# Optimization experiments

Measured on AMD Instinct MI355X. Metric: run time of the kernel, lower is better.

Reference implementation:

```python
import jax, jax.numpy as jnp
import numpy as np

WH = WW = 7          # window size
N_TOK = WH * WW      # 49 tokens per window
HEADS = 8
HEAD_DIM = 32
DIM = HEADS * HEAD_DIM  # 256
NW = 64              # windows per image (56x56 / 7x7)
BW = 64 * NW         # batch_images * windows = 4096


def _rel_pos_index(wh, ww):
    # Swin-style relative position index, flattened to (N*N,)
    coords = np.stack(np.meshgrid(np.arange(wh), np.arange(ww), indexing='ij'))  # (2, wh, ww)
    coords = coords.reshape(2, -1)                                               # (2, N)
    rel = coords[:, :, None] - coords[:, None, :]                                # (2, N, N)
    rel = rel.transpose(1, 2, 0).astype(np.int64)                                # (N, N, 2)
    rel[:, :, 0] += wh - 1
    rel[:, :, 1] += ww - 1
    rel[:, :, 0] *= 2 * ww - 1
    return jnp.asarray(rel.sum(-1).reshape(-1))                                  # (N*N,)

_REL_IDX = _rel_pos_index(WH, WW)


def setup_inputs() -> dict:
    key = jax.random.key(0)
    ks = jax.random.split(key, 5)
    x = jax.random.normal(ks[0], (BW, N_TOK, DIM), dtype=jnp.float32)
    mask = jnp.zeros((1, NW, 1, N_TOK, N_TOK), dtype=jnp.float32)
    w_qkv = jax.random.normal(ks[1], (DIM, 3 * HEADS * HEAD_DIM), dtype=jnp.float32) * 0.02
    b_qkv = jnp.zeros((3 * HEADS * HEAD_DIM,), dtype=jnp.float32)
    rel_table = jax.random.normal(ks[2], ((2 * WH - 1) * (2 * WW - 1), HEADS), dtype=jnp.float32) * 0.02
    w_out = jax.random.normal(ks[3], (HEADS * HEAD_DIM, DIM), dtype=jnp.float32) * 0.02
    b_out = jnp.zeros((DIM,), dtype=jnp.float32)
    return {"x": x, "mask": mask, "w_qkv": w_qkv, "b_qkv": b_qkv,
            "rel_table": rel_table, "w_out": w_out, "b_out": b_out}


def reference(x, mask, w_qkv, b_qkv, rel_table, w_out, b_out):
    bw, n, d = x.shape
    # QKV projection then split per original Rearrange:
    # 'b n (qkv h hd) -> qkv b h n hd'
    qkv = (x @ w_qkv + b_qkv).reshape(bw, n, 3, HEADS, HEAD_DIM)
    qkv = qkv.transpose(2, 0, 3, 1, 4)  # (3, bw, h, n, hd)
    q, k, v = qkv[0], qkv[1], qkv[2]
    # NOTE: original computes einsum('bnid,bnjd->bnij', k, q): a[i,j] = k_i . q_j
    a = jnp.einsum('bhid,bhjd->bhij', k, q) / jnp.sqrt(jnp.asarray(HEAD_DIM, x.dtype))
    # relative position bias: table gather then '(i j) h -> h i j'
    bias = rel_table[_REL_IDX].reshape(n, n, HEADS).transpose(2, 0, 1)  # (h, n, n)
    a = a + bias
    # mask add: '(b nW) h i j -> b nW h i j', + mask, back
    nw = mask.shape[1]
    a = a.reshape(bw // nw, nw, HEADS, n, n) + mask
    a = a.reshape(bw, HEADS, n, n)
    a = jax.nn.softmax(a, axis=-1)
    y = jnp.einsum('bhij,bhjd->bhid', a, v)        # (bw, h, n, hd)
    y = y.transpose(0, 2, 1, 3).reshape(bw, n, HEADS * HEAD_DIM)
    return y @ w_out + b_out
```

## Files before the change

kernel.cpp:

```cpp
#include <hip/hip_runtime.h>

typedef __attribute__((ext_vector_type(8))) short short8;
typedef __attribute__((ext_vector_type(4))) float f32x4;
typedef unsigned short u16;

#define NTOK 49
#define NBLK 4096

#define XF  0
#define QKP 16384
#define VTF 49152
#define MKF 65536
#define BQ  73728
#define BO  75264
#define POOL 75776

#define WS_WQT 0
#define WS_WOT 393216
#define WS_BIAS 524288

__device__ __forceinline__ u16 f2bf(float f) {
  unsigned u = __float_as_uint(f);
  return (u16)((u + 0x7fffu + ((u >> 16) & 1u)) >> 16);
}
__device__ __forceinline__ unsigned packbf(float a, float b) {
  return (unsigned)f2bf(a) | ((unsigned)f2bf(b) << 16);
}

__global__ void prep_kernel(const float* __restrict__ w_qkv,
                            const float* __restrict__ w_out,
                            const float* __restrict__ rel,
                            u16* __restrict__ wqTf,
                            u16* __restrict__ woTf,
                            float* __restrict__ biasf) {
  const int stride = gridDim.x * blockDim.x;
  const int gid = blockIdx.x * blockDim.x + threadIdx.x;
  for (int e = gid; e < 48 * 8 * 64 * 8; e += stride) {
    int eL = e & 7, ln = (e >> 3) & 63, ks = (e >> 9) & 7, ctg = e >> 12;
    int k = ks * 32 + (ln >> 4) * 8 + eL;
    int c = ctg * 16 + (ln & 15);
    wqTf[e] = f2bf(w_qkv[k * 768 + c]);
  }
  for (int e = gid; e < 16 * 8 * 64 * 8; e += stride) {
    int eL = e & 7, ln = (e >> 3) & 63, ks = (e >> 9) & 7, ctg = e >> 12;
    int k = ks * 32 + (ln >> 4) * 8 + eL;
    int c = ctg * 16 + (ln & 15);
    woTf[e] = f2bf(w_out[k * 256 + c]);
  }
  for (int e = gid; e < 8 * 16 * 64 * 4; e += stride) {
    int rg = e & 3, ln = (e >> 2) & 63, t = (e >> 8) & 15, h = e >> 12;
    int i = (t >> 2) * 16 + (ln & 15);
    int j = (t & 3) * 16 + (ln >> 4) * 4 + rg;
    float v;
    if (j >= NTOK) v = -1e30f;
    else if (i >= NTOK) v = 0.f;
    else {
      int dh = i / 7 - j / 7 + 6;
      int dw = i % 7 - j % 7 + 6;
      v = rel[(dh * 13 + dw) * 8 + h];
    }
    biasf[e] = v;
  }
}

__global__ void __launch_bounds__(512, 2) winattn_mfma(
    const float* __restrict__ x,
    const float* __restrict__ mask,
    const float* __restrict__ b_qkv,
    const float* __restrict__ b_out,
    const u16* __restrict__ wqTf,
    const u16* __restrict__ woTf,
    const float* __restrict__ biasf,
    float* __restrict__ out)
{
  __shared__ u16 pool[POOL];
  const int b = blockIdx.x, tid = threadIdx.x;
  const int lane = tid & 63, lo = lane & 15, hi = lane >> 4;
  const int w = tid >> 6;
  const f32x4 zf = {0.f, 0.f, 0.f, 0.f};
  float* mkf = (float*)(pool + MKF);
  float* bq  = (float*)(pool + BQ);
  float* bo  = (float*)(pool + BO);

  {
    const float4* xg = (const float4*)(x + (size_t)b * (NTOK * 256));
    for (int e = tid; e < 49 * 64; e += 512) {
      float4 v = xg[e];
      int r = e >> 6, c4 = (e & 63) << 2;
      int addr = (((r >> 4) * 8 + (c4 >> 5)) * 64 + ((c4 >> 3) & 3) * 16 + (r & 15)) * 8 + (c4 & 7);
      *(uint2*)&pool[XF + addr] = make_uint2(packbf(v.x, v.y), packbf(v.z, v.w));
    }
    for (int e = tid; e < 15 * 64; e += 512) {
      int r = 49 + (e >> 6), c4 = (e & 63) << 2;
      int addr = (((r >> 4) * 8 + (c4 >> 5)) * 64 + ((c4 >> 3) & 3) * 16 + (r & 15)) * 8 + (c4 & 7);
      *(uint2*)&pool[XF + addr] = make_uint2(0u, 0u);
    }
    const float* mrow = mask + (size_t)(b & 63) * (NTOK * NTOK);
    for (int e = tid; e < 4096; e += 512) {
      int rg = e & 3, l = (e >> 2) & 63, t = e >> 8;
      int i = (t >> 2) * 16 + (l & 15);
      int j = (t & 3) * 16 + (l >> 4) * 4 + rg;
      mkf[e] = (i < NTOK && j < NTOK) ? mrow[i * NTOK + j] : 0.f;
    }
    for (int e = tid; e < 768; e += 512) bq[e] = b_qkv[e];
    if (tid < 256) bo[tid] = b_out[tid];
  }
  __syncthreads();

  {
    const int ctg_[6] = {2*w, 2*w + 1, 16 + 2*w, 17 + 2*w, 32 + 2*w, 33 + 2*w};
    f32x4 acc[6][4];
    #pragma unroll
    for (int ct = 0; ct < 6; ++ct)
      #pragma unroll
      for (int rt = 0; rt < 4; ++rt) acc[ct][rt] = zf;
    #pragma unroll
    for (int ks = 0; ks < 8; ++ks) {
      short8 bx[4];
      #pragma unroll
      for (int rt = 0; rt < 4; ++rt)
        bx[rt] = *(const short8*)&pool[XF + ((rt * 8 + ks) * 64 + lane) * 8];
      #pragma unroll
      for (int ct = 0; ct < 6; ++ct) {
        short8 af = *(const short8*)&wqTf[((size_t)(ctg_[ct] * 8 + ks) * 64 + lane) * 8];
        #pragma unroll
        for (int rt = 0; rt < 4; ++rt)
          acc[ct][rt] = __builtin_amdgcn_mfma_f32_16x16x32_bf16(af, bx[rt], acc[ct][rt], 0, 0, 0);
      }
    }
    #pragma unroll
    for (int ct = 0; ct < 6; ++ct) {
      const int ctg = ctg_[ct];
      f32x4 bias = *(const f32x4*)&bq[ctg * 16 + hi * 4];
      #pragma unroll
      for (int rt = 0; rt < 4; ++rt) {
        f32x4 v = acc[ct][rt] + bias;
        if (ct < 4) {
          int hi2 = (ctg & 1) * 2 + (hi >> 1);
          int eb = (hi & 1) * 4;
          int base = QKP + w * 4096 + (ct >= 2 ? 2048 : 0);
          *(uint2*)&pool[base + (rt * 64 + hi2 * 16 + lo) * 8 + eb] =
              make_uint2(packbf(v[0], v[1]), packbf(v[2], v[3]));
        } else {
          int dblk = ctg & 1;
          int ks2 = rt >> 1;
          int hi2 = (rt & 1) * 2 + (lo >> 3);
          int e2 = lo & 7;
          int vb = VTF + w * 2048 + ((dblk * 2 + ks2) * 64 + hi2 * 16) * 8 + e2;
          pool[vb + (hi * 4 + 0) * 8] = f2bf(v[0]);
          pool[vb + (hi * 4 + 1) * 8] = f2bf(v[1]);
          pool[vb + (hi * 4 + 2) * 8] = f2bf(v[2]);
          pool[vb + (hi * 4 + 3) * 8] = f2bf(v[3]);
        }
      }
    }
  }
  __syncthreads();

  f32x4 sT[4][4];
  {
    short8 qa[4], ka[4];
    #pragma unroll
    for (int t2 = 0; t2 < 4; ++t2) {
      qa[t2] = *(const short8*)&pool[QKP + w * 4096 + (t2 * 64 + lane) * 8];
      ka[t2] = *(const short8*)&pool[QKP + w * 4096 + 2048 + (t2 * 64 + lane) * 8];
    }
    #pragma unroll
    for (int jt = 0; jt < 4; ++jt)
      #pragma unroll
      for (int it = 0; it < 4; ++it)
        sT[jt][it] = __builtin_amdgcn_mfma_f32_16x16x32_bf16(qa[jt], ka[it], zf, 0, 0, 0);
  }

  float inv[4];
  {
    const float* bh = biasf + ((size_t)w << 12);
    float rs[4] = {0.f, 0.f, 0.f, 0.f};
    #pragma unroll
    for (int jt = 0; jt < 4; ++jt) {
      #pragma unroll
      for (int it = 0; it < 4; ++it) {
        const int t = it * 4 + jt;
        f32x4 bm = *(const f32x4*)&bh[(t * 64 + lane) * 4];
        f32x4 mm = *(const f32x4*)&mkf[(t * 64 + lane) * 4];
        float p0 = __expf(fmaf(sT[jt][it][0], 0.17677669529663687f, bm[0] + mm[0]));
        float p1 = __expf(fmaf(sT[jt][it][1], 0.17677669529663687f, bm[1] + mm[1]));
        float p2 = __expf(fmaf(sT[jt][it][2], 0.17677669529663687f, bm[2] + mm[2]));
        float p3 = __expf(fmaf(sT[jt][it][3], 0.17677669529663687f, bm[3] + mm[3]));
        rs[it] += (p0 + p1) + (p2 + p3);
        int hi2 = (jt & 1) * 2 + (hi >> 1);
        int eb = (hi & 1) * 4;
        *(uint2*)&pool[QKP + w * 4096 + ((it * 2 + (jt >> 1)) * 64 + hi2 * 16 + lo) * 8 + eb] =
            make_uint2(packbf(p0, p1), packbf(p2, p3));
      }
    }
    #pragma unroll
    for (int it = 0; it < 4; ++it) {
      float r2 = rs[it] + __shfl_xor(rs[it], 16);
      float r4 = r2 + __shfl_xor(r2, 32);
      inv[it] = 1.f / r4;
    }
  }

  {
    short8 va[2][2];
    #pragma unroll
    for (int dblk = 0; dblk < 2; ++dblk)
      #pragma unroll
      for (int k2 = 0; k2 < 2; ++k2)
        va[dblk][k2] = *(const short8*)&pool[VTF + w * 2048 + ((dblk * 2 + k2) * 64 + lane) * 8];
    f32x4 ya[2][4];
    #pragma unroll
    for (int it = 0; it < 4; ++it) { ya[0][it] = zf; ya[1][it] = zf; }
    #pragma unroll
    for (int it = 0; it < 4; ++it)
      #pragma unroll
      for (int k2 = 0; k2 < 2; ++k2) {
        short8 pb = *(const short8*)&pool[QKP + w * 4096 + ((it * 2 + k2) * 64 + lane) * 8];
        ya[0][it] = __builtin_amdgcn_mfma_f32_16x16x32_bf16(va[0][k2], pb, ya[0][it], 0, 0, 0);
        ya[1][it] = __builtin_amdgcn_mfma_f32_16x16x32_bf16(va[1][k2], pb, ya[1][it], 0, 0, 0);
      }
    #pragma unroll
    for (int it = 0; it < 4; ++it) {
      #pragma unroll
      for (int dblk = 0; dblk < 2; ++dblk) {
        float y0 = ya[dblk][it][0] * inv[it];
        float y1 = ya[dblk][it][1] * inv[it];
        float y2 = ya[dblk][it][2] * inv[it];
        float y3 = ya[dblk][it][3] * inv[it];
        int hi2 = dblk * 2 + (hi >> 1);
        int eb = (hi & 1) * 4;
        *(uint2*)&pool[XF + ((it * 8 + w) * 64 + hi2 * 16 + lo) * 8 + eb] =
            make_uint2(packbf(y0, y1), packbf(y2, y3));
      }
    }
  }
  __syncthreads();

  {
    f32x4 pacc[2][4];
    #pragma unroll
    for (int ct = 0; ct < 2; ++ct)
      #pragma unroll
      for (int rt = 0; rt < 4; ++rt) pacc[ct][rt] = zf;
    #pragma unroll
    for (int ks = 0; ks < 8; ++ks) {
      short8 yb[4];
      #pragma unroll
      for (int rt = 0; rt < 4; ++rt)
        yb[rt] = *(const short8*)&pool[XF + ((rt * 8 + ks) * 64 + lane) * 8];
      #pragma unroll
      for (int ct = 0; ct < 2; ++ct) {
        short8 wf = *(const short8*)&woTf[((size_t)((w * 2 + ct) * 8 + ks) * 64 + lane) * 8];
        #pragma unroll
        for (int rt = 0; rt < 4; ++rt)
          pacc[ct][rt] = __builtin_amdgcn_mfma_f32_16x16x32_bf16(wf, yb[rt], pacc[ct][rt], 0, 0, 0);
      }
    }
    float* og = out + (size_t)b * (NTOK * 256);
    #pragma unroll
    for (int ct = 0; ct < 2; ++ct) {
      const int cb = (w * 2 + ct) * 16 + hi * 4;
      f32x4 bb = *(const f32x4*)&bo[cb];
      #pragma unroll
      for (int rt = 0; rt < 4; ++rt) {
        const int r = rt * 16 + lo;
        if (r < NTOK) {
          f32x4 vv = pacc[ct][rt] + bb;
          *(f32x4*)(og + (size_t)r * 256 + cb) = vv;
        }
      }
    }
  }
}

extern "C" void kernel_launch(void* const* d_in, const int* in_sizes, int n_in,
                              void* d_out, int out_size, void* d_ws, size_t ws_size,
                              hipStream_t stream) {
  const float *x = nullptr, *mask = nullptr, *w_qkv = nullptr, *b_qkv = nullptr,
              *rel_t = nullptr, *w_out = nullptr, *b_out = nullptr;
  for (int i = 0; i < n_in; ++i) {
    const float* p = (const float*)d_in[i];
    switch (in_sizes[i]) {
      case 4096 * 49 * 256: x = p; break;
      case 64 * 49 * 49:    mask = p; break;
      case 256 * 768:       w_qkv = p; break;
      case 768:             b_qkv = p; break;
      case 169 * 8:         rel_t = p; break;
      case 256 * 256:       w_out = p; break;
      case 256:             b_out = p; break;
    }
  }
  char* wsb = (char*)d_ws;
  u16* wqTf = (u16*)(wsb + WS_WQT);
  u16* woTf = (u16*)(wsb + WS_WOT);
  float* biasf = (float*)(wsb + WS_BIAS);

  hipLaunchKernelGGL(prep_kernel, dim3(512), dim3(256), 0, stream,
                     w_qkv, w_out, rel_t, wqTf, woTf, biasf);
  hipLaunchKernelGGL(winattn_mfma, dim3(NBLK), dim3(512), 0, stream,
                     x, mask, b_qkv, b_out, wqTf, woTf, biasf, (float*)d_out);
}
```

Baseline: 346.4 us.

## Use 16 waves per block, splitting attention by head and query-tile halves

Doubles the block to 1024 threads. The QKV projection is spread over 16 waves (3 column tiles each), and each head's attention is split across two waves by query-tile pairs. Softmax probabilities now stay in registers and are reshuffled with cross-lane shuffles instead of a round trip through LDS. The output projection also gives one column tile per wave. The aim is more parallelism per window and lower per-wave register pressure, at the cost of extra shuffle instructions and a launch-bounds request of 4 blocks of 1024 threads that the LDS use likely cannot meet.

```diff
diff --git a/kernel.cpp b/kernel.cpp
--- a/kernel.cpp
+++ b/kernel.cpp
@@ -48,7 +48,7 @@
     woTf[e] = f2bf(w_out[k * 256 + c]);
   }
   for (int e = gid; e < 8 * 16 * 64 * 4; e += stride) {
-    int rg = e & 3, ln = (e >> 2) & 63, t = (e >> 8) & 15, h = e >> 12;
+    int rg = e & 3, ln = (e >> 2) & 63, t = (e >> 8) & 15, hh = e >> 12;
     int i = (t >> 2) * 16 + (ln & 15);
     int j = (t & 3) * 16 + (ln >> 4) * 4 + rg;
     float v;
@@ -57,13 +57,13 @@
     else {
       int dh = i / 7 - j / 7 + 6;
       int dw = i % 7 - j % 7 + 6;
-      v = rel[(dh * 13 + dw) * 8 + h];
+      v = rel[(dh * 13 + dw) * 8 + hh];
     }
     biasf[e] = v;
   }
 }
 
-__global__ void __launch_bounds__(512, 2) winattn_mfma(
+__global__ void __launch_bounds__(1024, 4) winattn_mfma(
     const float* __restrict__ x,
     const float* __restrict__ mask,
     const float* __restrict__ b_qkv,
@@ -77,6 +77,8 @@
   const int b = blockIdx.x, tid = threadIdx.x;
   const int lane = tid & 63, lo = lane & 15, hi = lane >> 4;
   const int w = tid >> 6;
+  const int h = w & 7;
+  const int it0 = (w >> 3) * 2;
   const f32x4 zf = {0.f, 0.f, 0.f, 0.f};
   float* mkf = (float*)(pool + MKF);
   float* bq  = (float*)(pool + BQ);
@@ -84,34 +86,34 @@
 
   {
     const float4* xg = (const float4*)(x + (size_t)b * (NTOK * 256));
-    for (int e = tid; e < 49 * 64; e += 512) {
+    for (int e = tid; e < 49 * 64; e += 1024) {
       float4 v = xg[e];
       int r = e >> 6, c4 = (e & 63) << 2;
       int addr = (((r >> 4) * 8 + (c4 >> 5)) * 64 + ((c4 >> 3) & 3) * 16 + (r & 15)) * 8 + (c4 & 7);
       *(uint2*)&pool[XF + addr] = make_uint2(packbf(v.x, v.y), packbf(v.z, v.w));
     }
-    for (int e = tid; e < 15 * 64; e += 512) {
+    if (tid < 15 * 64) {
+      int e = tid;
       int r = 49 + (e >> 6), c4 = (e & 63) << 2;
       int addr = (((r >> 4) * 8 + (c4 >> 5)) * 64 + ((c4 >> 3) & 3) * 16 + (r & 15)) * 8 + (c4 & 7);
       *(uint2*)&pool[XF + addr] = make_uint2(0u, 0u);
     }
     const float* mrow = mask + (size_t)(b & 63) * (NTOK * NTOK);
-    for (int e = tid; e < 4096; e += 512) {
+    for (int e = tid; e < 4096; e += 1024) {
       int rg = e & 3, l = (e >> 2) & 63, t = e >> 8;
       int i = (t >> 2) * 16 + (l & 15);
       int j = (t & 3) * 16 + (l >> 4) * 4 + rg;
       mkf[e] = (i < NTOK && j < NTOK) ? mrow[i * NTOK + j] : 0.f;
     }
-    for (int e = tid; e < 768; e += 512) bq[e] = b_qkv[e];
+    if (tid < 768) bq[tid] = b_qkv[tid];
     if (tid < 256) bo[tid] = b_out[tid];
   }
   __syncthreads();
 
   {
-    const int ctg_[6] = {2*w, 2*w + 1, 16 + 2*w, 17 + 2*w, 32 + 2*w, 33 + 2*w};
-    f32x4 acc[6][4];
-    #pragma unroll
-    for (int ct = 0; ct < 6; ++ct)
+    f32x4 acc[3][4];
+    #pragma unroll
+    for (int ct = 0; ct < 3; ++ct)
       #pragma unroll
       for (int rt = 0; rt < 4; ++rt) acc[ct][rt] = zf;
     #pragma unroll
@@ -121,24 +123,25 @@
       for (int rt = 0; rt < 4; ++rt)
         bx[rt] = *(const short8*)&pool[XF + ((rt * 8 + ks) * 64 + lane) * 8];
       #pragma unroll
-      for (int ct = 0; ct < 6; ++ct) {
-        short8 af = *(const short8*)&wqTf[((size_t)(ctg_[ct] * 8 + ks) * 64 + lane) * 8];
+      for (int ct = 0; ct < 3; ++ct) {
+        short8 af = *(const short8*)&wqTf[((size_t)((3 * w + ct) * 8 + ks) * 64 + lane) * 8];
         #pragma unroll
         for (int rt = 0; rt < 4; ++rt)
           acc[ct][rt] = __builtin_amdgcn_mfma_f32_16x16x32_bf16(af, bx[rt], acc[ct][rt], 0, 0, 0);
       }
     }
     #pragma unroll
-    for (int ct = 0; ct < 6; ++ct) {
-      const int ctg = ctg_[ct];
+    for (int ct = 0; ct < 3; ++ct) {
+      const int ctg = 3 * w + ct;
+      const int head2 = (ctg & 15) >> 1;
       f32x4 bias = *(const f32x4*)&bq[ctg * 16 + hi * 4];
       #pragma unroll
       for (int rt = 0; rt < 4; ++rt) {
         f32x4 v = acc[ct][rt] + bias;
-        if (ct < 4) {
+        if (ctg < 32) {
+          int base = QKP + head2 * 4096 + (ctg >= 16 ? 2048 : 0);
           int hi2 = (ctg & 1) * 2 + (hi >> 1);
           int eb = (hi & 1) * 4;
-          int base = QKP + w * 4096 + (ct >= 2 ? 2048 : 0);
           *(uint2*)&pool[base + (rt * 64 + hi2 * 16 + lo) * 8 + eb] =
               make_uint2(packbf(v[0], v[1]), packbf(v[2], v[3]));
         } else {
@@ -146,7 +149,7 @@
           int ks2 = rt >> 1;
           int hi2 = (rt & 1) * 2 + (lo >> 3);
           int e2 = lo & 7;
-          int vb = VTF + w * 2048 + ((dblk * 2 + ks2) * 64 + hi2 * 16) * 8 + e2;
+          int vb = VTF + head2 * 2048 + ((dblk * 2 + ks2) * 64 + hi2 * 16) * 8 + e2;
           pool[vb + (hi * 4 + 0) * 8] = f2bf(v[0]);
           pool[vb + (hi * 4 + 1) * 8] = f2bf(v[1]);
           pool[vb + (hi * 4 + 2) * 8] = f2bf(v[2]);
@@ -157,49 +160,49 @@
   }
   __syncthreads();
 
-  f32x4 sT[4][4];
-  {
-    short8 qa[4], ka[4];
-    #pragma unroll
-    for (int t2 = 0; t2 < 4; ++t2) {
-      qa[t2] = *(const short8*)&pool[QKP + w * 4096 + (t2 * 64 + lane) * 8];
-      ka[t2] = *(const short8*)&pool[QKP + w * 4096 + 2048 + (t2 * 64 + lane) * 8];
-    }
-    #pragma unroll
-    for (int jt = 0; jt < 4; ++jt)
-      #pragma unroll
-      for (int it = 0; it < 4; ++it)
-        sT[jt][it] = __builtin_amdgcn_mfma_f32_16x16x32_bf16(qa[jt], ka[it], zf, 0, 0, 0);
-  }
-
-  float inv[4];
-  {
-    const float* bh = biasf + ((size_t)w << 12);
-    float rs[4] = {0.f, 0.f, 0.f, 0.f};
+  float rs0 = 0.f, rs1 = 0.f;
+  unsigned pkp[4][2][2];
+  {
+    short8 ka0 = *(const short8*)&pool[QKP + h * 4096 + 2048 + ((it0 + 0) * 64 + lane) * 8];
+    short8 ka1 = *(const short8*)&pool[QKP + h * 4096 + 2048 + ((it0 + 1) * 64 + lane) * 8];
+    const float* bh = biasf + ((size_t)h << 12);
     #pragma unroll
     for (int jt = 0; jt < 4; ++jt) {
-      #pragma unroll
-      for (int it = 0; it < 4; ++it) {
-        const int t = it * 4 + jt;
+      short8 qa = *(const short8*)&pool[QKP + h * 4096 + (jt * 64 + lane) * 8];
+      f32x4 s0 = __builtin_amdgcn_mfma_f32_16x16x32_bf16(qa, ka0, zf, 0, 0, 0);
+      f32x4 s1 = __builtin_amdgcn_mfma_f32_16x16x32_bf16(qa, ka1, zf, 0, 0, 0);
+      {
+        const int t = (it0 + 0) * 4 + jt;
         f32x4 bm = *(const f32x4*)&bh[(t * 64 + lane) * 4];
         f32x4 mm = *(const f32x4*)&mkf[(t * 64 + lane) * 4];
-        float p0 = __expf(fmaf(sT[jt][it][0], 0.17677669529663687f, bm[0] + mm[0]));
-        float p1 = __expf(fmaf(sT[jt][it][1], 0.17677669529663687f, bm[1] + mm[1]));
-        float p2 = __expf(fmaf(sT[jt][it][2], 0.17677669529663687f, bm[2] + mm[2]));
-        float p3 = __expf(fmaf(sT[jt][it][3], 0.17677669529663687f, bm[3] + mm[3]));
-        rs[it] += (p0 + p1) + (p2 + p3);
-        int hi2 = (jt & 1) * 2 + (hi >> 1);
-        int eb = (hi & 1) * 4;
-        *(uint2*)&pool[QKP + w * 4096 + ((it * 2 + (jt >> 1)) * 64 + hi2 * 16 + lo) * 8 + eb] =
-            make_uint2(packbf(p0, p1), packbf(p2, p3));
-      }
-    }
-    #pragma unroll
-    for (int it = 0; it < 4; ++it) {
-      float r2 = rs[it] + __shfl_xor(rs[it], 16);
-      float r4 = r2 + __shfl_xor(r2, 32);
-      inv[it] = 1.f / r4;
-    }
+        float p0 = __expf(fmaf(s0[0], 0.17677669529663687f, bm[0] + mm[0]));
+        float p1 = __expf(fmaf(s0[1], 0.17677669529663687f, bm[1] + mm[1]));
+        float p2 = __expf(fmaf(s0[2], 0.17677669529663687f, bm[2] + mm[2]));
+        float p3 = __expf(fmaf(s0[3], 0.17677669529663687f, bm[3] + mm[3]));
+        rs0 += (p0 + p1) + (p2 + p3);
+        pkp[jt][0][0] = packbf(p0, p1);
+        pkp[jt][0][1] = packbf(p2, p3);
+      }
+      {
+        const int t = (it0 + 1) * 4 + jt;
+        f32x4 bm = *(const f32x4*)&bh[(t * 64 + lane) * 4];
+        f32x4 mm = *(const f32x4*)&mkf[(t * 64 + lane) * 4];
+        float p0 = __expf(fmaf(s1[0], 0.17677669529663687f, bm[0] + mm[0]));
+        float p1 = __expf(fmaf(s1[1], 0.17677669529663687f, bm[1] + mm[1]));
+        float p2 = __expf(fmaf(s1[2], 0.17677669529663687f, bm[2] + mm[2]));
+        float p3 = __expf(fmaf(s1[3], 0.17677669529663687f, bm[3] + mm[3]));
+        rs1 += (p0 + p1) + (p2 + p3);
+        pkp[jt][1][0] = packbf(p0, p1);
+        pkp[jt][1][1] = packbf(p2, p3);
+      }
+    }
+  }
+  float inv0, inv1;
+  {
+    float r2 = rs0 + __shfl_xor(rs0, 16);
+    inv0 = 1.f / (r2 + __shfl_xor(r2, 32));
+    float r3 = rs1 + __shfl_xor(rs1, 16);
+    inv1 = 1.f / (r3 + __shfl_xor(r3, 32));
   }
 
   {
@@ -208,29 +211,44 @@
     for (int dblk = 0; dblk < 2; ++dblk)
       #pragma unroll
       for (int k2 = 0; k2 < 2; ++k2)
-        va[dblk][k2] = *(const short8*)&pool[VTF + w * 2048 + ((dblk * 2 + k2) * 64 + lane) * 8];
-    f32x4 ya[2][4];
-    #pragma unroll
-    for (int it = 0; it < 4; ++it) { ya[0][it] = zf; ya[1][it] = zf; }
-    #pragma unroll
-    for (int it = 0; it < 4; ++it)
+        va[dblk][k2] = *(const short8*)&pool[VTF + h * 2048 + ((dblk * 2 + k2) * 64 + lane) * 8];
+    f32x4 ya[2][2];
+    ya[0][0] = zf; ya[0][1] = zf; ya[1][0] = zf; ya[1][1] = zf;
+    const int src0 = lo + ((hi & 1) * 2) * 16;
+    const int src1 = src0 + 16;
+    const bool hiSel = (hi & 2) != 0;
+    #pragma unroll
+    for (int itL = 0; itL < 2; ++itL)
       #pragma unroll
       for (int k2 = 0; k2 < 2; ++k2) {
-        short8 pb = *(const short8*)&pool[QKP + w * 4096 + ((it * 2 + k2) * 64 + lane) * 8];
-        ya[0][it] = __builtin_amdgcn_mfma_f32_16x16x32_bf16(va[0][k2], pb, ya[0][it], 0, 0, 0);
-        ya[1][it] = __builtin_amdgcn_mfma_f32_16x16x32_bf16(va[1][k2], pb, ya[1][it], 0, 0, 0);
-      }
-    #pragma unroll
-    for (int it = 0; it < 4; ++it) {
+        unsigned a0 = (unsigned)__shfl((int)pkp[2 * k2][itL][0], src0);
+        unsigned b0 = (unsigned)__shfl((int)pkp[2 * k2 + 1][itL][0], src0);
+        unsigned a1 = (unsigned)__shfl((int)pkp[2 * k2][itL][1], src0);
+        unsigned b1 = (unsigned)__shfl((int)pkp[2 * k2 + 1][itL][1], src0);
+        unsigned a2 = (unsigned)__shfl((int)pkp[2 * k2][itL][0], src1);
+        unsigned b2 = (unsigned)__shfl((int)pkp[2 * k2 + 1][itL][0], src1);
+        unsigned a3 = (unsigned)__shfl((int)pkp[2 * k2][itL][1], src1);
+        unsigned b3 = (unsigned)__shfl((int)pkp[2 * k2 + 1][itL][1], src1);
+        union { unsigned u[4]; short8 s8; } pb;
+        pb.u[0] = hiSel ? b0 : a0;
+        pb.u[1] = hiSel ? b1 : a1;
+        pb.u[2] = hiSel ? b2 : a2;
+        pb.u[3] = hiSel ? b3 : a3;
+        ya[0][itL] = __builtin_amdgcn_mfma_f32_16x16x32_bf16(va[0][k2], pb.s8, ya[0][itL], 0, 0, 0);
+        ya[1][itL] = __builtin_amdgcn_mfma_f32_16x16x32_bf16(va[1][k2], pb.s8, ya[1][itL], 0, 0, 0);
+      }
+    #pragma unroll
+    for (int itL = 0; itL < 2; ++itL) {
+      const float inv = itL ? inv1 : inv0;
       #pragma unroll
       for (int dblk = 0; dblk < 2; ++dblk) {
-        float y0 = ya[dblk][it][0] * inv[it];
-        float y1 = ya[dblk][it][1] * inv[it];
-        float y2 = ya[dblk][it][2] * inv[it];
-        float y3 = ya[dblk][it][3] * inv[it];
+        float y0 = ya[dblk][itL][0] * inv;
+        float y1 = ya[dblk][itL][1] * inv;
+        float y2 = ya[dblk][itL][2] * inv;
+        float y3 = ya[dblk][itL][3] * inv;
         int hi2 = dblk * 2 + (hi >> 1);
         int eb = (hi & 1) * 4;
-        *(uint2*)&pool[XF + ((it * 8 + w) * 64 + hi2 * 16 + lo) * 8 + eb] =
+        *(uint2*)&pool[XF + (((it0 + itL) * 8 + h) * 64 + hi2 * 16 + lo) * 8 + eb] =
             make_uint2(packbf(y0, y1), packbf(y2, y3));
       }
     }
@@ -238,37 +256,26 @@
   __syncthreads();
 
   {
-    f32x4 pacc[2][4];
-    #pragma unroll
-    for (int ct = 0; ct < 2; ++ct)
-      #pragma unroll
-      for (int rt = 0; rt < 4; ++rt) pacc[ct][rt] = zf;
+    f32x4 pacc[4];
+    pacc[0] = zf; pacc[1] = zf; pacc[2] = zf; pacc[3] = zf;
     #pragma unroll
     for (int ks = 0; ks < 8; ++ks) {
-      short8 yb[4];
-      #pragma unroll
-      for (int rt = 0; rt < 4; ++rt)
-        yb[rt] = *(const short8*)&pool[XF + ((rt * 8 + ks) * 64 + lane) * 8];
-      #pragma unroll
-      for (int ct = 0; ct < 2; ++ct) {
-        short8 wf = *(const short8*)&woTf[((size_t)((w * 2 + ct) * 8 + ks) * 64 + lane) * 8];
-        #pragma unroll
-        for (int rt = 0; rt < 4; ++rt)
-          pacc[ct][rt] = __builtin_amdgcn_mfma_f32_16x16x32_bf16(wf, yb[rt], pacc[ct][rt], 0, 0, 0);
+      short8 wf = *(const short8*)&woTf[((size_t)(w * 8 + ks) * 64 + lane) * 8];
+      #pragma unroll
+      for (int rt = 0; rt < 4; ++rt) {
+        short8 yb = *(const short8*)&pool[XF + ((rt * 8 + ks) * 64 + lane) * 8];
+        pacc[rt] = __builtin_amdgcn_mfma_f32_16x16x32_bf16(wf, yb, pacc[rt], 0, 0, 0);
       }
     }
     float* og = out + (size_t)b * (NTOK * 256);
-    #pragma unroll
-    for (int ct = 0; ct < 2; ++ct) {
-      const int cb = (w * 2 + ct) * 16 + hi * 4;
-      f32x4 bb = *(const f32x4*)&bo[cb];
-      #pragma unroll
-      for (int rt = 0; rt < 4; ++rt) {
-        const int r = rt * 16 + lo;
-        if (r < NTOK) {
-          f32x4 vv = pacc[ct][rt] + bb;
-          *(f32x4*)(og + (size_t)r * 256 + cb) = vv;
-        }
+    const int cb = w * 16 + hi * 4;
+    f32x4 bb = *(const f32x4*)&bo[cb];
+    #pragma unroll
+    for (int rt = 0; rt < 4; ++rt) {
+      const int r = rt * 16 + lo;
+      if (r < NTOK) {
+        f32x4 vv = pacc[rt] + bb;
+        *(f32x4*)(og + (size_t)r * 256 + cb) = vv;
       }
     }
   }
@@ -298,6 +305,6 @@
 
   hipLaunchKernelGGL(prep_kernel, dim3(512), dim3(256), 0, stream,
                      w_qkv, w_out, rel_t, wqTf, woTf, biasf);
-  hipLaunchKernelGGL(winattn_mfma, dim3(NBLK), dim3(512), 0, stream,
+  hipLaunchKernelGGL(winattn_mfma, dim3(NBLK), dim3(1024), 0, stream,
                      x, mask, b_qkv, b_out, wqTf, woTf, biasf, (float*)d_out);
 }
```

Measured after the change: 290.0 us. -16.3%, faster.

## Keep Q/K/P in registers via lane shuffles and shrink LDS for higher occupancy

Applied to the files above, without the earlier changes.

Q and K stay in registers and are rearranged into MFMA operand layout with cross-lane shuffles, and the softmax probabilities are handled the same way. This removes the Q/K/P shared-memory round trips and one barrier. The per-window mask is pre-laid-out in a workspace buffer by the prep kernel, and the biases are read straight from global memory, so LDS shrinks from about 148KB to 64KB and launch bounds rise to 4 blocks per CU. In exchange it adds many shuffle instructions and puts more register pressure under the tighter occupancy target, which could cause spills.

```diff
diff --git a/kernel.cpp b/kernel.cpp
--- a/kernel.cpp
+++ b/kernel.cpp
@@ -7,17 +7,14 @@
 #define NTOK 49
 #define NBLK 4096
 
-#define XF  0
-#define QKP 16384
-#define VTF 49152
-#define MKF 65536
-#define BQ  73728
-#define BO  75264
-#define POOL 75776
+#define XF 0
+#define VY 16384
+#define POOLN 32768
 
 #define WS_WQT 0
 #define WS_WOT 393216
 #define WS_BIAS 524288
+#define WS_MKG 655360
 
 __device__ __forceinline__ u16 f2bf(float f) {
   unsigned u = __float_as_uint(f);
@@ -27,12 +24,33 @@
   return (unsigned)f2bf(a) | ((unsigned)f2bf(b) << 16);
 }
 
+__device__ __forceinline__ short8 asm_frag(unsigned c0p0, unsigned c0p1,
+                                           unsigned c1p0, unsigned c1p1,
+                                           int srcA, int srcB, bool cSel) {
+  unsigned a0 = (unsigned)__shfl((int)c0p0, srcA);
+  unsigned b0 = (unsigned)__shfl((int)c1p0, srcA);
+  unsigned a1 = (unsigned)__shfl((int)c0p1, srcA);
+  unsigned b1 = (unsigned)__shfl((int)c1p1, srcA);
+  unsigned a2 = (unsigned)__shfl((int)c0p0, srcB);
+  unsigned b2 = (unsigned)__shfl((int)c1p0, srcB);
+  unsigned a3 = (unsigned)__shfl((int)c0p1, srcB);
+  unsigned b3 = (unsigned)__shfl((int)c1p1, srcB);
+  union { unsigned u[4]; short8 s8; } r;
+  r.u[0] = cSel ? b0 : a0;
+  r.u[1] = cSel ? b1 : a1;
+  r.u[2] = cSel ? b2 : a2;
+  r.u[3] = cSel ? b3 : a3;
+  return r.s8;
+}
+
 __global__ void prep_kernel(const float* __restrict__ w_qkv,
                             const float* __restrict__ w_out,
                             const float* __restrict__ rel,
+                            const float* __restrict__ mask,
                             u16* __restrict__ wqTf,
                             u16* __restrict__ woTf,
-                            float* __restrict__ biasf) {
+                            float* __restrict__ biasf,
+                            float* __restrict__ mkg) {
   const int stride = gridDim.x * blockDim.x;
   const int gid = blockIdx.x * blockDim.x + threadIdx.x;
   for (int e = gid; e < 48 * 8 * 64 * 8; e += stride) {
@@ -48,7 +66,7 @@
     woTf[e] = f2bf(w_out[k * 256 + c]);
   }
   for (int e = gid; e < 8 * 16 * 64 * 4; e += stride) {
-    int rg = e & 3, ln = (e >> 2) & 63, t = (e >> 8) & 15, h = e >> 12;
+    int rg = e & 3, ln = (e >> 2) & 63, t = (e >> 8) & 15, hh = e >> 12;
     int i = (t >> 2) * 16 + (ln & 15);
     int j = (t & 3) * 16 + (ln >> 4) * 4 + rg;
     float v;
@@ -57,30 +75,33 @@
     else {
       int dh = i / 7 - j / 7 + 6;
       int dw = i % 7 - j % 7 + 6;
-      v = rel[(dh * 13 + dw) * 8 + h];
+      v = rel[(dh * 13 + dw) * 8 + hh];
     }
     biasf[e] = v;
   }
-}
-
-__global__ void __launch_bounds__(512, 2) winattn_mfma(
+  for (int e = gid; e < 64 * 16 * 64 * 4; e += stride) {
+    int rg = e & 3, ln = (e >> 2) & 63, t = (e >> 8) & 15, wdw = e >> 12;
+    int i = (t >> 2) * 16 + (ln & 15);
+    int j = (t & 3) * 16 + (ln >> 4) * 4 + rg;
+    mkg[e] = (i < NTOK && j < NTOK) ? mask[wdw * (NTOK * NTOK) + i * NTOK + j] : 0.f;
+  }
+}
+
+__global__ void __launch_bounds__(512, 4) winattn_mfma(
     const float* __restrict__ x,
-    const float* __restrict__ mask,
     const float* __restrict__ b_qkv,
     const float* __restrict__ b_out,
     const u16* __restrict__ wqTf,
     const u16* __restrict__ woTf,
     const float* __restrict__ biasf,
+    const float* __restrict__ mkg,
     float* __restrict__ out)
 {
-  __shared__ u16 pool[POOL];
+  __shared__ u16 pool[POOLN];
   const int b = blockIdx.x, tid = threadIdx.x;
   const int lane = tid & 63, lo = lane & 15, hi = lane >> 4;
-  const int w = tid >> 6;
+  const int h = tid >> 6;
   const f32x4 zf = {0.f, 0.f, 0.f, 0.f};
-  float* mkf = (float*)(pool + MKF);
-  float* bq  = (float*)(pool + BQ);
-  float* bo  = (float*)(pool + BO);
 
   {
     const float4* xg = (const float4*)(x + (size_t)b * (NTOK * 256));
@@ -95,23 +116,15 @@
       int addr = (((r >> 4) * 8 + (c4 >> 5)) * 64 + ((c4 >> 3) & 3) * 16 + (r & 15)) * 8 + (c4 & 7);
       *(uint2*)&pool[XF + addr] = make_uint2(0u, 0u);
     }
-    const float* mrow = mask + (size_t)(b & 63) * (NTOK * NTOK);
-    for (int e = tid; e < 4096; e += 512) {
-      int rg = e & 3, l = (e >> 2) & 63, t = e >> 8;
-      int i = (t >> 2) * 16 + (l & 15);
-      int j = (t & 3) * 16 + (l >> 4) * 4 + rg;
-      mkf[e] = (i < NTOK && j < NTOK) ? mrow[i * NTOK + j] : 0.f;
-    }
-    for (int e = tid; e < 768; e += 512) bq[e] = b_qkv[e];
-    if (tid < 256) bo[tid] = b_out[tid];
   }
   __syncthreads();
 
-  {
-    const int ctg_[6] = {2*w, 2*w + 1, 16 + 2*w, 17 + 2*w, 32 + 2*w, 33 + 2*w};
-    f32x4 acc[6][4];
-    #pragma unroll
-    for (int ct = 0; ct < 6; ++ct)
+  unsigned pq[2][4][2], pk[2][4][2];
+  {
+    const int ctgA[3] = {2 * h, 2 * h + 1, 16 + 2 * h};
+    f32x4 acc[3][4];
+    #pragma unroll
+    for (int ct = 0; ct < 3; ++ct)
       #pragma unroll
       for (int rt = 0; rt < 4; ++rt) acc[ct][rt] = zf;
     #pragma unroll
@@ -121,32 +134,58 @@
       for (int rt = 0; rt < 4; ++rt)
         bx[rt] = *(const short8*)&pool[XF + ((rt * 8 + ks) * 64 + lane) * 8];
       #pragma unroll
-      for (int ct = 0; ct < 6; ++ct) {
-        short8 af = *(const short8*)&wqTf[((size_t)(ctg_[ct] * 8 + ks) * 64 + lane) * 8];
+      for (int ct = 0; ct < 3; ++ct) {
+        short8 af = *(const short8*)&wqTf[((size_t)(ctgA[ct] * 8 + ks) * 64 + lane) * 8];
         #pragma unroll
         for (int rt = 0; rt < 4; ++rt)
           acc[ct][rt] = __builtin_amdgcn_mfma_f32_16x16x32_bf16(af, bx[rt], acc[ct][rt], 0, 0, 0);
       }
     }
     #pragma unroll
-    for (int ct = 0; ct < 6; ++ct) {
-      const int ctg = ctg_[ct];
-      f32x4 bias = *(const f32x4*)&bq[ctg * 16 + hi * 4];
+    for (int ct = 0; ct < 3; ++ct) {
+      f32x4 bias = *(const f32x4*)(b_qkv + ctgA[ct] * 16 + hi * 4);
       #pragma unroll
       for (int rt = 0; rt < 4; ++rt) {
         f32x4 v = acc[ct][rt] + bias;
-        if (ct < 4) {
-          int hi2 = (ctg & 1) * 2 + (hi >> 1);
-          int eb = (hi & 1) * 4;
-          int base = QKP + w * 4096 + (ct >= 2 ? 2048 : 0);
-          *(uint2*)&pool[base + (rt * 64 + hi2 * 16 + lo) * 8 + eb] =
-              make_uint2(packbf(v[0], v[1]), packbf(v[2], v[3]));
-        } else {
-          int dblk = ctg & 1;
-          int ks2 = rt >> 1;
+        if (ct < 2) { pq[ct][rt][0] = packbf(v[0], v[1]); pq[ct][rt][1] = packbf(v[2], v[3]); }
+        else        { pk[0][rt][0]  = packbf(v[0], v[1]); pk[0][rt][1]  = packbf(v[2], v[3]); }
+      }
+    }
+  }
+  {
+    const int ctgB[3] = {17 + 2 * h, 32 + 2 * h, 33 + 2 * h};
+    f32x4 acc[3][4];
+    #pragma unroll
+    for (int ct = 0; ct < 3; ++ct)
+      #pragma unroll
+      for (int rt = 0; rt < 4; ++rt) acc[ct][rt] = zf;
+    #pragma unroll
+    for (int ks = 0; ks < 8; ++ks) {
+      short8 bx[4];
+      #pragma unroll
+      for (int rt = 0; rt < 4; ++rt)
+        bx[rt] = *(const short8*)&pool[XF + ((rt * 8 + ks) * 64 + lane) * 8];
+      #pragma unroll
+      for (int ct = 0; ct < 3; ++ct) {
+        short8 af = *(const short8*)&wqTf[((size_t)(ctgB[ct] * 8 + ks) * 64 + lane) * 8];
+        #pragma unroll
+        for (int rt = 0; rt < 4; ++rt)
+          acc[ct][rt] = __builtin_amdgcn_mfma_f32_16x16x32_bf16(af, bx[rt], acc[ct][rt], 0, 0, 0);
+      }
+    }
+    #pragma unroll
+    for (int ct = 0; ct < 3; ++ct) {
+      f32x4 bias = *(const f32x4*)(b_qkv + ctgB[ct] * 16 + hi * 4);
+      #pragma unroll
+      for (int rt = 0; rt < 4; ++rt) {
+        f32x4 v = acc[ct][rt] + bias;
+        if (ct == 0) { pk[1][rt][0] = packbf(v[0], v[1]); pk[1][rt][1] = packbf(v[2], v[3]); }
+        else {
+          const int dblk = ct - 1;
+          int k2 = rt >> 1;
           int hi2 = (rt & 1) * 2 + (lo >> 3);
           int e2 = lo & 7;
-          int vb = VTF + w * 2048 + ((dblk * 2 + ks2) * 64 + hi2 * 16) * 8 + e2;
+          int vb = VY + ((dblk * 2 + k2) * 8 + h) * 512 + (hi2 * 16) * 8 + e2;
           pool[vb + (hi * 4 + 0) * 8] = f2bf(v[0]);
           pool[vb + (hi * 4 + 1) * 8] = f2bf(v[1]);
           pool[vb + (hi * 4 + 2) * 8] = f2bf(v[2]);
@@ -155,83 +194,70 @@
       }
     }
   }
-  __syncthreads();
-
-  f32x4 sT[4][4];
-  {
-    short8 qa[4], ka[4];
-    #pragma unroll
-    for (int t2 = 0; t2 < 4; ++t2) {
-      qa[t2] = *(const short8*)&pool[QKP + w * 4096 + (t2 * 64 + lane) * 8];
-      ka[t2] = *(const short8*)&pool[QKP + w * 4096 + 2048 + (t2 * 64 + lane) * 8];
-    }
-    #pragma unroll
-    for (int jt = 0; jt < 4; ++jt)
-      #pragma unroll
-      for (int it = 0; it < 4; ++it)
-        sT[jt][it] = __builtin_amdgcn_mfma_f32_16x16x32_bf16(qa[jt], ka[it], zf, 0, 0, 0);
-  }
-
-  float inv[4];
-  {
-    const float* bh = biasf + ((size_t)w << 12);
-    float rs[4] = {0.f, 0.f, 0.f, 0.f};
+
+  const int srcA = lo + 32 * (hi & 1);
+  const int srcB = srcA + 16;
+  const bool cSel = hi >= 2;
+  unsigned pkp[4][4][2];
+  float rs[4] = {0.f, 0.f, 0.f, 0.f};
+  {
+    short8 ka[4];
+    #pragma unroll
+    for (int it = 0; it < 4; ++it)
+      ka[it] = asm_frag(pk[0][it][0], pk[0][it][1], pk[1][it][0], pk[1][it][1], srcA, srcB, cSel);
+    const float* bh = biasf + h * 4096;
+    const float* mh = mkg + (size_t)(b & 63) * 4096;
     #pragma unroll
     for (int jt = 0; jt < 4; ++jt) {
+      short8 qa = asm_frag(pq[0][jt][0], pq[0][jt][1], pq[1][jt][0], pq[1][jt][1], srcA, srcB, cSel);
       #pragma unroll
       for (int it = 0; it < 4; ++it) {
+        f32x4 st = __builtin_amdgcn_mfma_f32_16x16x32_bf16(qa, ka[it], zf, 0, 0, 0);
         const int t = it * 4 + jt;
         f32x4 bm = *(const f32x4*)&bh[(t * 64 + lane) * 4];
-        f32x4 mm = *(const f32x4*)&mkf[(t * 64 + lane) * 4];
-        float p0 = __expf(fmaf(sT[jt][it][0], 0.17677669529663687f, bm[0] + mm[0]));
-        float p1 = __expf(fmaf(sT[jt][it][1], 0.17677669529663687f, bm[1] + mm[1]));
-        float p2 = __expf(fmaf(sT[jt][it][2], 0.17677669529663687f, bm[2] + mm[2]));
-        float p3 = __expf(fmaf(sT[jt][it][3], 0.17677669529663687f, bm[3] + mm[3]));
+        f32x4 mm = *(const f32x4*)&mh[(t * 64 + lane) * 4];
+        float p0 = __expf(fmaf(st[0], 0.17677669529663687f, bm[0] + mm[0]));
+        float p1 = __expf(fmaf(st[1], 0.17677669529663687f, bm[1] + mm[1]));
+        float p2 = __expf(fmaf(st[2], 0.17677669529663687f, bm[2] + mm[2]));
+        float p3 = __expf(fmaf(st[3], 0.17677669529663687f, bm[3] + mm[3]));
         rs[it] += (p0 + p1) + (p2 + p3);
-        int hi2 = (jt & 1) * 2 + (hi >> 1);
-        int eb = (hi & 1) * 4;
-        *(uint2*)&pool[QKP + w * 4096 + ((it * 2 + (jt >> 1)) * 64 + hi2 * 16 + lo) * 8 + eb] =
-            make_uint2(packbf(p0, p1), packbf(p2, p3));
-      }
-    }
+        pkp[jt][it][0] = packbf(p0, p1);
+        pkp[jt][it][1] = packbf(p2, p3);
+      }
+    }
+  }
+  float inv[4];
+  #pragma unroll
+  for (int it = 0; it < 4; ++it) {
+    float r2 = rs[it] + __shfl_xor(rs[it], 16);
+    inv[it] = 1.f / (r2 + __shfl_xor(r2, 32));
+  }
+
+  {
+    short8 va[2][2];
+    #pragma unroll
+    for (int dblk = 0; dblk < 2; ++dblk)
+      #pragma unroll
+      for (int k2 = 0; k2 < 2; ++k2)
+        va[dblk][k2] = *(const short8*)&pool[VY + ((dblk * 2 + k2) * 8 + h) * 512 + lane * 8];
     #pragma unroll
     for (int it = 0; it < 4; ++it) {
-      float r2 = rs[it] + __shfl_xor(rs[it], 16);
-      float r4 = r2 + __shfl_xor(r2, 32);
-      inv[it] = 1.f / r4;
-    }
-  }
-
-  {
-    short8 va[2][2];
-    #pragma unroll
-    for (int dblk = 0; dblk < 2; ++dblk)
-      #pragma unroll
-      for (int k2 = 0; k2 < 2; ++k2)
-        va[dblk][k2] = *(const short8*)&pool[VTF + w * 2048 + ((dblk * 2 + k2) * 64 + lane) * 8];
-    f32x4 ya[2][4];
-    #pragma unroll
-    for (int it = 0; it < 4; ++it) { ya[0][it] = zf; ya[1][it] = zf; }
-    #pragma unroll
-    for (int it = 0; it < 4; ++it)
+      f32x4 y0 = zf, y1 = zf;
       #pragma unroll
       for (int k2 = 0; k2 < 2; ++k2) {
-        short8 pb = *(const short8*)&pool[QKP + w * 4096 + ((it * 2 + k2) * 64 + lane) * 8];
-        ya[0][it] = __builtin_amdgcn_mfma_f32_16x16x32_bf16(va[0][k2], pb, ya[0][it], 0, 0, 0);
-        ya[1][it] = __builtin_amdgcn_mfma_f32_16x16x32_bf16(va[1][k2], pb, ya[1][it], 0, 0, 0);
-      }
-    #pragma unroll
-    for (int it = 0; it < 4; ++it) {
+        short8 pb = asm_frag(pkp[2 * k2][it][0], pkp[2 * k2][it][1],
+                             pkp[2 * k2 + 1][it][0], pkp[2 * k2 + 1][it][1], srcA, srcB, cSel);
+        y0 = __builtin_amdgcn_mfma_f32_16x16x32_bf16(va[0][k2], pb, y0, 0, 0, 0);
+        y1 = __builtin_amdgcn_mfma_f32_16x16x32_bf16(va[1][k2], pb, y1, 0, 0, 0);
+      }
+      const float iv = inv[it];
       #pragma unroll
       for (int dblk = 0; dblk < 2; ++dblk) {
-        float y0 = ya[dblk][it][0] * inv[it];
-        float y1 = ya[dblk][it][1] * inv[it];
-        float y2 = ya[dblk][it][2] * inv[it];
-        float y3 = ya[dblk][it][3] * inv[it];
+        f32x4 yy = dblk ? y1 : y0;
         int hi2 = dblk * 2 + (hi >> 1);
         int eb = (hi & 1) * 4;
-        *(uint2*)&pool[XF + ((it * 8 + w) * 64 + hi2 * 16 + lo) * 8 + eb] =
-            make_uint2(packbf(y0, y1), packbf(y2, y3));
+        *(uint2*)&pool[VY + (it * 8 + h) * 512 + (hi2 * 16 + lo) * 8 + eb] =
+            make_uint2(packbf(yy[0] * iv, yy[1] * iv), packbf(yy[2] * iv, yy[3] * iv));
       }
     }
   }
@@ -248,10 +274,10 @@
       short8 yb[4];
       #pragma unroll
       for (int rt = 0; rt < 4; ++rt)
-        yb[rt] = *(const short8*)&pool[XF + ((rt * 8 + ks) * 64 + lane) * 8];
+        yb[rt] = *(const short8*)&pool[VY + (rt * 8 + ks) * 512 + lane * 8];
       #pragma unroll
       for (int ct = 0; ct < 2; ++ct) {
-        short8 wf = *(const short8*)&woTf[((size_t)((w * 2 + ct) * 8 + ks) * 64 + lane) * 8];
+        short8 wf = *(const short8*)&woTf[((size_t)((h * 2 + ct) * 8 + ks) * 64 + lane) * 8];
         #pragma unroll
         for (int rt = 0; rt < 4; ++rt)
           pacc[ct][rt] = __builtin_amdgcn_mfma_f32_16x16x32_bf16(wf, yb[rt], pacc[ct][rt], 0, 0, 0);
@@ -260,8 +286,8 @@
     float* og = out + (size_t)b * (NTOK * 256);
     #pragma unroll
     for (int ct = 0; ct < 2; ++ct) {
-      const int cb = (w * 2 + ct) * 16 + hi * 4;
-      f32x4 bb = *(const f32x4*)&bo[cb];
+      const int cb = (h * 2 + ct) * 16 + hi * 4;
+      f32x4 bb = *(const f32x4*)(b_out + cb);
       #pragma unroll
       for (int rt = 0; rt < 4; ++rt) {
         const int r = rt * 16 + lo;
@@ -292,12 +318,13 @@
     }
   }
   char* wsb = (char*)d_ws;
-  u16* wqTf = (u16*)(wsb + WS_WQT);
-  u16* woTf = (u16*)(wsb + WS_WOT);
+  u16* wqTf   = (u16*)(wsb + WS_WQT);
+  u16* woTf   = (u16*)(wsb + WS_WOT);
   float* biasf = (float*)(wsb + WS_BIAS);
-
-  hipLaunchKernelGGL(prep_kernel, dim3(512), dim3(256), 0, stream,
-                     w_qkv, w_out, rel_t, wqTf, woTf, biasf);
+  float* mkg   = (float*)(wsb + WS_MKG);
+
+  hipLaunchKernelGGL(prep_kernel, dim3(1024), dim3(256), 0, stream,
+                     w_qkv, w_out, rel_t, mask, wqTf, woTf, biasf, mkg);
   hipLaunchKernelGGL(winattn_mfma, dim3(NBLK), dim3(512), 0, stream,
-                     x, mask, b_qkv, b_out, wqTf, woTf, biasf, (float*)d_out);
-}
+                     x, b_qkv, b_out, wqTf, woTf, biasf, mkg, (float*)d_out);
+}
```

Result: slower. 832.9 us (+140.4%).
